# Kernel tuning notes

Hardware: AMD Instinct MI355X
Metric: run time of the kernel (lower is better)

The kernel has to match this reference:

```python
import jax, jax.numpy as jnp
import numpy as np
import math

V = 32000      # vocab_size
D = 1024       # hidden_dims
T_MAX = 1024   # max_txt_len
L = 4          # n_layers
H = 8          # heads (fixed in CausalMHA)
HD = D // H
B, T = 2, 1024
EPS = 1e-5


def setup_inputs() -> dict:
    key = jax.random.key(0)
    ks = jax.random.split(key, 20)
    s = 0.02
    inp = {
        "x": jax.random.randint(ks[0], (B, T), 0, V, dtype=jnp.int64) if jax.config.read("jax_enable_x64") else jax.random.randint(ks[0], (B, T), 0, V, dtype=jnp.int32),
        "tok_emb": jax.random.normal(ks[1], (V, D), jnp.float32) * s,
        "pos_emb": jax.random.normal(ks[2], (1, T_MAX, D), jnp.float32) * s,
        "ln1_g": jnp.ones((L, D), jnp.float32),
        "ln1_b": jnp.zeros((L, D), jnp.float32),
        "wqkv": jax.random.normal(ks[3], (L, D, 3 * D), jnp.float32) * s,
        "bqkv": jnp.zeros((L, 3 * D), jnp.float32),
        "wo": jax.random.normal(ks[4], (L, D, D), jnp.float32) * s,
        "bo": jnp.zeros((L, D), jnp.float32),
        "ln2_g": jnp.ones((L, D), jnp.float32),
        "ln2_b": jnp.zeros((L, D), jnp.float32),
        "wfc": jax.random.normal(ks[5], (L, D, 4 * D), jnp.float32) * s,   # no bias
        "wfc2": jax.random.normal(ks[6], (L, 4 * D, D), jnp.float32) * s,  # no bias
        "fn_g": jnp.ones((D,), jnp.float32),
        "fn_b": jnp.zeros((D,), jnp.float32),
        "wout": jax.random.normal(ks[7], (D, V), jnp.float32) * s,
        "bout": jnp.zeros((V,), jnp.float32),
    }
    return inp


def _ln(x, g, b):
    mu = jnp.mean(x, axis=-1, keepdims=True)
    var = jnp.var(x, axis=-1, keepdims=True)
    return (x - mu) * jax.lax.rsqrt(var + EPS) * g + b


def _attn(xn, wqkv_l, bqkv_l, wo_l, bo_l):
    Bb, Tt, _ = xn.shape
    qkv = xn @ wqkv_l + bqkv_l                      # [B,T,3D]
    q, k, v = jnp.split(qkv, 3, axis=-1)
    q = q.reshape(Bb, Tt, H, HD)
    k = k.reshape(Bb, Tt, H, HD)
    v = v.reshape(Bb, Tt, H, HD)
    scores = jnp.einsum("bqhd,bkhd->bhqk", q, k) / math.sqrt(HD)
    mask = jnp.triu(jnp.ones((Tt, Tt), bool), k=1)   # True above diagonal
    scores = jnp.where(mask, jnp.float32(-jnp.inf), scores)
    att = jax.nn.softmax(scores, axis=-1)
    out = jnp.einsum("bhqk,bkhd->bqhd", att, v).reshape(Bb, Tt, D)
    return out @ wo_l + bo_l


def reference(x, tok_emb, pos_emb, ln1_g, ln1_b, wqkv, bqkv, wo, bo,
              ln2_g, ln2_b, wfc, wfc2, fn_g, fn_b, wout, bout):
    Tt = x.shape[1]
    h = tok_emb[x] + pos_emb[:, :Tt, :]              # [B,T,D]
    for i in range(L):
        h = h + _attn(_ln(h, ln1_g[i], ln1_b[i]), wqkv[i], bqkv[i], wo[i], bo[i])
        hn = _ln(h, ln2_g[i], ln2_b[i])
        h = h + jax.nn.gelu(hn @ wfc[i], approximate=False) @ wfc2[i]
    h = _ln(h, fn_g, fn_b)
    return h @ wout + bout                           # [B,T,V] logits
```

## Files before the change

### kernel.cpp

```cpp
#include <hip/hip_runtime.h>
#include <math.h>
#include <stdint.h>

#define D_  1024
#define T_  1024
#define H_  8
#define HD_ 128
#define L_  4
#define V_  32000
#define M_  2048

typedef __attribute__((ext_vector_type(4))) float f32x4;
typedef __attribute__((ext_vector_type(4))) short s16x4;
typedef __attribute__((ext_vector_type(8))) short s16x8;
typedef unsigned short u16;

__device__ __forceinline__ u16 f2bf(float f) {
  union { float f; uint32_t u; } c; c.f = f;
  uint32_t r = c.u + 0x7fffu + ((c.u >> 16) & 1u);
  return (u16)(r >> 16);
}
__device__ __forceinline__ float bf2f(u16 h) {
  union { uint32_t u; float f; } c; c.u = ((uint32_t)h) << 16;
  return c.f;
}
__device__ __forceinline__ float gelu_f(float x) {
  return 0.5f * x * (1.0f + erff(x * 0.70710678118654752f));
}

__device__ __forceinline__ void gload16(const u16* g, u16* l) {
  __builtin_amdgcn_global_load_lds(
      (const __attribute__((address_space(1))) void*)(uintptr_t)g,
      (__attribute__((address_space(3))) void*)(uint32_t)(uintptr_t)l,
      16, 0, 0);
}

__device__ __forceinline__ void convT_f32_tile(const float* __restrict__ in,
                                               u16* __restrict__ out,
                                               int ldin, int ldout,
                                               int c0, int r0,
                                               u16 (*tile)[72])
{
  const int t = threadIdx.x;
  const int rr = t >> 2, cs = (t & 3) << 4;
  u16 tmp[16];
  const float* p = in + (size_t)(r0 + rr) * ldin + c0 + cs;
#pragma unroll
  for (int q = 0; q < 4; ++q) {
    f32x4 v = *(const f32x4*)(p + q * 4);
#pragma unroll
    for (int j = 0; j < 4; ++j) tmp[q * 4 + j] = f2bf(v[j]);
  }
  *(s16x8*)&tile[rr][cs]     = *(const s16x8*)tmp;
  *(s16x8*)&tile[rr][cs + 8] = *(const s16x8*)(tmp + 8);
  __syncthreads();
  const int cr = t >> 2, rs = (t & 3) << 4;
  u16 o[16];
#pragma unroll
  for (int j = 0; j < 16; ++j) o[j] = tile[rs + j][cr];
  u16* op = out + (size_t)(c0 + cr) * ldout + r0 + rs;
  *(s16x8*)op       = *(const s16x8*)o;
  *(s16x8*)(op + 8) = *(const s16x8*)(o + 8);
}

template<int INF32>
__global__ __launch_bounds__(256)
void convT_kernel(const void* __restrict__ inv, u16* __restrict__ out,
                  int ldin, int ldout, long inZ, long outZ)
{
  __shared__ __align__(16) u16 tile[64][72];
  const int c0 = blockIdx.x << 6, r0 = blockIdx.y << 6;
  if (INF32) {
    convT_f32_tile((const float*)inv + (size_t)blockIdx.z * inZ,
                   out + (size_t)blockIdx.z * outZ, ldin, ldout, c0, r0, tile);
    return;
  }
  const int t = threadIdx.x;
  const int rr = t >> 2, cs = (t & 3) << 4;
  const u16* in = (const u16*)inv + (size_t)blockIdx.z * inZ;
  const u16* p = in + (size_t)(r0 + rr) * ldin + c0 + cs;
  s16x8 v0 = *(const s16x8*)(p);
  s16x8 v1 = *(const s16x8*)(p + 8);
  *(s16x8*)&tile[rr][cs]     = v0;
  *(s16x8*)&tile[rr][cs + 8] = v1;
  __syncthreads();
  const int cr = t >> 2, rs = (t & 3) << 4;
  u16 o[16];
#pragma unroll
  for (int j = 0; j < 16; ++j) o[j] = tile[rs + j][cr];
  u16* op = out + (size_t)blockIdx.z * outZ + (size_t)(c0 + cr) * ldout + r0 + rs;
  *(s16x8*)op       = *(const s16x8*)o;
  *(s16x8*)(op + 8) = *(const s16x8*)(o + 8);
}

__global__ __launch_bounds__(256)
void conv4_kernel(const float* __restrict__ wqkv_l, const float* __restrict__ wo_l,
                  const float* __restrict__ wfc_l, const float* __restrict__ wfc2_l,
                  u16* __restrict__ Wq, u16* __restrict__ Wo,
                  u16* __restrict__ Wf1, u16* __restrict__ Wf2)
{
  __shared__ __align__(16) u16 tile[64][72];
  int f = blockIdx.x;
  if (f < 768) {
    convT_f32_tile(wqkv_l, Wq, 3 * D_, D_, (f % 48) << 6, (f / 48) << 6, tile);
  } else if (f < 1024) {
    f -= 768;
    convT_f32_tile(wo_l, Wo, D_, D_, (f & 15) << 6, (f >> 4) << 6, tile);
  } else if (f < 2048) {
    f -= 1024;
    convT_f32_tile(wfc_l, Wf1, 4 * D_, D_, (f & 63) << 6, (f >> 6) << 6, tile);
  } else {
    f -= 2048;
    convT_f32_tile(wfc2_l, Wf2, D_, 4 * D_, (f & 15) << 6, (f >> 4) << 6, tile);
  }
}

template<int TM, int ACT, int BIAS, int OUT>
__device__ __forceinline__
void gemm2_body(const u16* __restrict__ A, const u16* __restrict__ Bw,
                const float* __restrict__ bias, const float* __restrict__ res,
                void* __restrict__ Cv,
                int K, int lda, int ldb, int ldc, float scale,
                int bx, int by)
{
  constexpr int WN  = (TM == 128) ? 2 : 4;
  constexpr int WNW = 128 / WN;
  constexpr int NJ  = WNW / 16;
  constexpr int AR  = TM / 64;

  const int m0 = bx * TM, n0 = by * 128;
  const int ktiles = K >> 5;

  __shared__ __align__(16) u16 As[2][TM * 32];
  __shared__ __align__(16) u16 Bs[2][128 * 32];

  const int tid = threadIdx.x, lane = tid & 63, wave = tid >> 6;
  const int wm = wave / WN, wn = wave % WN;
  const int l15 = lane & 15, l4 = lane >> 4;
  const int srow = lane >> 2, scol = (lane & 3) << 3;

  f32x4 acc[4][NJ];
  const f32x4 z4 = {0.f, 0.f, 0.f, 0.f};
#pragma unroll
  for (int i = 0; i < 4; ++i)
#pragma unroll
    for (int j = 0; j < NJ; ++j) acc[i][j] = z4;

  auto stage = [&](int kt, int buf) {
    const int kc = (kt << 5) + scol;
#pragma unroll
    for (int r = 0; r < AR; ++r) {
      const int row = r * 64 + wave * 16;
      gload16(A + (size_t)(m0 + row + srow) * lda + kc, &As[buf][row * 32]);
    }
#pragma unroll
    for (int r = 0; r < 2; ++r) {
      const int row = r * 64 + wave * 16;
      gload16(Bw + (size_t)(n0 + row + srow) * ldb + kc, &Bs[buf][row * 32]);
    }
  };

  stage(0, 0);
  __syncthreads();

  for (int kt = 0; kt < ktiles; ++kt) {
    const int buf = kt & 1;
    if (kt + 1 < ktiles) stage(kt + 1, buf ^ 1);
    const u16* ap = &As[buf][(wm * 64 + l15) * 32 + (l4 << 3)];
    const u16* bp = &Bs[buf][(wn * WNW + l15) * 32 + (l4 << 3)];
    s16x8 af[4], bf[NJ];
#pragma unroll
    for (int i = 0; i < 4; ++i) af[i] = *(const s16x8*)(ap + i * (16 * 32));
#pragma unroll
    for (int j = 0; j < NJ; ++j) bf[j] = *(const s16x8*)(bp + j * (16 * 32));
#pragma unroll
    for (int i = 0; i < 4; ++i)
#pragma unroll
      for (int j = 0; j < NJ; ++j)
        acc[i][j] = __builtin_amdgcn_mfma_f32_16x16x32_bf16(af[i], bf[j], acc[i][j], 0, 0, 0);
    __syncthreads();
  }

  float* Cf = (float*)Cv;
  u16*   Ch = (u16*)Cv;
#pragma unroll
  for (int i = 0; i < 4; ++i) {
    const int row0 = m0 + wm * 64 + i * 16 + l4 * 4;
#pragma unroll
    for (int j = 0; j < NJ; ++j) {
      const int col = n0 + wn * WNW + j * 16 + l15;
      const float bv = BIAS ? bias[col] : 0.0f;
#pragma unroll
      for (int r = 0; r < 4; ++r) {
        float v = acc[i][j][r] * scale + bv;
        if (ACT) v = gelu_f(v);
        const size_t idx = (size_t)(row0 + r) * ldc + col;
        if (OUT == 0)      Ch[idx] = f2bf(v);
        else if (OUT == 1) Cf[idx] = v;
        else               Cf[idx] = v + res[idx];
      }
    }
  }
}

__device__ __forceinline__ int2 swz2d() {
  const int gx = gridDim.x, gy = gridDim.y;
  int flat = blockIdx.y * gx + blockIdx.x;
  const int nwg = gx * gy;
  int swz = (flat & 7) * (nwg >> 3) + (flat >> 3);
  return make_int2(swz % gx, swz / gx);
}

__global__ __launch_bounds__(256)
void gemm_qkv(const u16* A, const u16* Bw, const float* bias, void* Cv) {
  int2 b = swz2d();
  gemm2_body<128, 0, 1, 0>(A, Bw, bias, nullptr, Cv, D_, D_, D_, 3 * D_, 1.0f, b.x, b.y);
}
__global__ __launch_bounds__(256)
void gemm_fc1(const u16* A, const u16* Bw, void* Cv) {
  int2 b = swz2d();
  gemm2_body<128, 1, 0, 0>(A, Bw, nullptr, nullptr, Cv, D_, D_, D_, 4 * D_, 1.0f, b.x, b.y);
}
__global__ __launch_bounds__(256)
void gemm_wo(const u16* A, const u16* Bw, const float* bias, const float* res,
             void* Cv) {
  int2 b = swz2d();
  gemm2_body<64, 0, 1, 2>(A, Bw, bias, res, Cv, D_, D_, D_, D_, 1.0f, b.x, b.y);
}
__global__ __launch_bounds__(256)
void gemm_fc2s(const u16* __restrict__ A, const u16* __restrict__ Bw,
               float* __restrict__ P) {
  const int gx = gridDim.x, gy = gridDim.y;
  int flat = (blockIdx.z * gy + blockIdx.y) * gx + blockIdx.x;
  const int nwg = gx * gy * gridDim.z;
  int swz = (flat & 7) * (nwg >> 3) + (flat >> 3);
  const int bx = swz % gx; swz /= gx;
  const int by = swz % gy;
  const int z  = swz / gy;
  gemm2_body<64, 0, 0, 1>(A + z * 1024, Bw + z * 1024, nullptr, nullptr,
                          P + (size_t)z * M_ * D_,
                          1024, 4 * D_, 4 * D_, D_, 1.0f, bx, by);
}
__global__ __launch_bounds__(256)
void reduce4_kernel(const float* __restrict__ P, float* __restrict__ h) {
  const size_t i = (size_t)blockIdx.x * D_ + threadIdx.x * 4;
  f32x4 a = *(const f32x4*)&h[i];
#pragma unroll
  for (int z = 0; z < 4; ++z) {
    f32x4 p = *(const f32x4*)&P[(size_t)z * M_ * D_ + i];
    a[0] += p[0]; a[1] += p[1]; a[2] += p[2]; a[3] += p[3];
  }
  *(f32x4*)&h[i] = a;
}

__global__ __launch_bounds__(512, 2)
void gemm8_logits(const u16* __restrict__ A, const u16* __restrict__ Bw,
                  const float* __restrict__ bias, float* __restrict__ C)
{
  int flat = blockIdx.x;
  int swz = (flat & 7) * 125 + (flat >> 3);
  const int bx = swz & 7;
  const int by = swz >> 3;
  const int m0 = bx << 8, n0 = by << 8;

  __shared__ __align__(16) u16 lds[65536];

  const int tid = threadIdx.x, lane = tid & 63, wave = tid >> 6;
  const int wm = wave >> 2, wn = wave & 3;
  const int l15 = lane & 15, l4 = lane >> 4;

  f32x4 acc[8][4];
  const f32x4 z4 = {0.f, 0.f, 0.f, 0.f};
#pragma unroll
  for (int i = 0; i < 8; ++i)
#pragma unroll
    for (int j = 0; j < 4; ++j) acc[i][j] = z4;

  auto stg = [&](const u16* G, int rowbase, int slot, int kt, int kh) {
    kt = (kt < 15) ? kt : 15;
#pragma unroll
    for (int r = 0; r < 2; ++r) {
      const int u = r * 512 + (wave << 6) + lane;
      const int rw = u >> 2, ks = u & 3;
      const int ksw = ks ^ ((rw >> 1) & 3);
      const u16* src = G + (size_t)(rowbase + rw) * 1024 + (kt << 6) + (kh << 5) + (ksw << 3);
      gload16(src, &lds[slot + r * 4096 + (wave << 9)]);
    }
  };

  s16x8 af[4], bfr[4];

#define LDA4(bb, kk, mh)                                                      \
  {                                                                           \
    _Pragma("unroll") for (int f = 0; f < 4; ++f) {                           \
      const int rw = wm * 128 + (mh) * 64 + f * 16 + l15;                     \
      af[f] = *(const s16x8*)&lds[(bb) + (kk) * 8192 + rw * 32 +              \
                                  ((l4 ^ ((rw >> 1) & 3)) << 3)];             \
    }                                                                         \
  }
#define LDB4(bb, kk)                                                          \
  {                                                                           \
    _Pragma("unroll") for (int f = 0; f < 4; ++f) {                           \
      const int rn = wn * 64 + f * 16 + l15;                                  \
      bfr[f] = *(const s16x8*)&lds[(bb) + 16384 + (kk) * 8192 + rn * 32 +     \
                                   ((l4 ^ ((rn >> 1) & 3)) << 3)];            \
    }                                                                         \
  }
#define MFMA16(mh)                                                            \
  {                                                                           \
    __builtin_amdgcn_s_barrier();                                             \
    asm volatile("s_waitcnt lgkmcnt(0)" ::: "memory");                        \
    __builtin_amdgcn_sched_barrier(0);                                        \
    __builtin_amdgcn_s_setprio(1);                                            \
    _Pragma("unroll") for (int f = 0; f < 4; ++f)                             \
      _Pragma("unroll") for (int nf = 0; nf < 4; ++nf)                        \
        acc[(mh) * 4 + f][nf] = __builtin_amdgcn_mfma_f32_16x16x32_bf16(      \
            af[f], bfr[nf], acc[(mh) * 4 + f][nf], 0, 0, 0);                  \
    __builtin_amdgcn_s_setprio(0);                                            \
  }
#define BAR() __builtin_amdgcn_s_barrier()
#define VM4() asm volatile("s_waitcnt vmcnt(4)" ::: "memory")

  stg(A,  m0, 0,             0, 0);
  stg(Bw, n0, 16384,         0, 0);
  stg(A,  m0, 8192,          0, 1);
  stg(Bw, n0, 16384 + 8192,  0, 1);
  stg(A,  m0, 32768,         1, 0);
  stg(Bw, n0, 32768 + 16384, 1, 0);
  VM4();
  BAR();

  for (int i = 0; i < 8; ++i) {
    const int t = 2 * i;
    LDA4(0, 0, 0); LDB4(0, 0);
    stg(A, m0, 32768 + 8192, t + 1, 1);
    MFMA16(0); BAR();
    LDA4(0, 0, 1);
    stg(Bw, n0, 32768 + 24576, t + 1, 1);
    MFMA16(1); BAR();
    LDA4(0, 1, 0); LDB4(0, 1);
    stg(A, m0, 0, t + 2, 0);
    MFMA16(0); BAR();
    LDA4(0, 1, 1);
    stg(Bw, n0, 16384, t + 2, 0);
    MFMA16(1); VM4(); BAR();
    LDA4(32768, 0, 0); LDB4(32768, 0);
    stg(A, m0, 8192, t + 2, 1);
    MFMA16(0); BAR();
    LDA4(32768, 0, 1);
    stg(Bw, n0, 16384 + 8192, t + 2, 1);
    MFMA16(1); BAR();
    LDA4(32768, 1, 0); LDB4(32768, 1);
    stg(A, m0, 32768, t + 3, 0);
    MFMA16(0); BAR();
    LDA4(32768, 1, 1);
    stg(Bw, n0, 32768 + 16384, t + 3, 0);
    MFMA16(1); VM4(); BAR();
  }
#undef LDA4
#undef LDB4
#undef MFMA16
#undef BAR
#undef VM4

  float bv[4];
#pragma unroll
  for (int nf = 0; nf < 4; ++nf) bv[nf] = bias[n0 + wn * 64 + nf * 16 + l15];
#pragma unroll
  for (int mf = 0; mf < 8; ++mf) {
    const int row0 = m0 + wm * 128 + mf * 16 + l4 * 4;
#pragma unroll
    for (int nf = 0; nf < 4; ++nf) {
      const int col = n0 + wn * 64 + nf * 16 + l15;
#pragma unroll
      for (int r = 0; r < 4; ++r)
        C[(size_t)(row0 + r) * V_ + col] = acc[mf][nf][r] + bv[nf];
    }
  }
}

__global__ __launch_bounds__(256)
void flash_attn(const u16* __restrict__ qkv, const u16* __restrict__ Vt,
                u16* __restrict__ xo)
{
  const int qb = 15 - blockIdx.x;
  const int z  = blockIdx.y;
  const int b  = z >> 3, hh = z & 7;

  __shared__ __align__(16) u16 Ks[64 * 128];
  __shared__ __align__(16) u16 Vs[128 * 64];
  __shared__ __align__(16) u16 Ps[64 * 80];

  const int tid = threadIdx.x, lane = tid & 63, w = tid >> 6;
  const int l15 = lane & 15, l4 = lane >> 4;
  const float iscale = 0.08838834764831845f;

  const int qrow = qb * 64 + w * 16 + l15;
  const u16* qptr = qkv + ((size_t)(b * T_) + qrow) * (3 * D_) + hh * HD_;

  s16x8 bQ[4];
#pragma unroll
  for (int ks = 0; ks < 4; ++ks)
    bQ[ks] = *(const s16x8*)(qptr + ks * 32 + l4 * 8);

  f32x4 O[8];
#pragma unroll
  for (int i = 0; i < 8; ++i) O[i] = {0.f, 0.f, 0.f, 0.f};
  float m_run = -1e30f, l_run = 0.f;

  const int ntiles = qb + 1;
  for (int kt = 0; kt < ntiles; ++kt) {
    __syncthreads();
    {
      const int r = tid >> 2, c = (tid & 3) << 5;
      const u16* src = qkv + ((size_t)(b * T_) + kt * 64 + r) * (3 * D_) + D_ + hh * HD_ + c;
#pragma unroll
      for (int u = 0; u < 4; ++u) {
        s16x8 v = *(const s16x8*)(src + u * 8);
        const int dblk = (c >> 3) + u;
        *(s16x8*)&Ks[r * 128 + ((dblk ^ (r & 7)) << 3)] = v;
      }
      const int d = tid >> 1, kc0 = (tid & 1) << 5;
      const u16* vsrc = Vt + ((size_t)z * HD_ + d) * T_ + kt * 64 + kc0;
#pragma unroll
      for (int u = 0; u < 4; ++u) {
        s16x8 v = *(const s16x8*)(vsrc + u * 8);
        const int kblk = (kc0 >> 3) + u;
        *(s16x8*)&Vs[d * 64 + ((kblk ^ (d & 7)) << 3)] = v;
      }
    }
    __syncthreads();

    f32x4 st[4];
#pragma unroll
    for (int mf = 0; mf < 4; ++mf) st[mf] = {0.f, 0.f, 0.f, 0.f};
#pragma unroll
    for (int ks = 0; ks < 4; ++ks) {
      s16x8 aK[4];
#pragma unroll
      for (int mf = 0; mf < 4; ++mf) {
        const int r = mf * 16 + l15;
        aK[mf] = *(const s16x8*)&Ks[r * 128 + ((((ks << 2) + l4) ^ (r & 7)) << 3)];
      }
#pragma unroll
      for (int mf = 0; mf < 4; ++mf)
        st[mf] = __builtin_amdgcn_mfma_f32_16x16x32_bf16(aK[mf], bQ[ks], st[mf], 0, 0, 0);
    }

    const bool diag = (kt == qb);
    float sv[16];
    float mx = -1e30f;
#pragma unroll
    for (int mf = 0; mf < 4; ++mf)
#pragma unroll
      for (int r = 0; r < 4; ++r) {
        float s = st[mf][r] * iscale;
        if (diag) {
          const int k = kt * 64 + mf * 16 + l4 * 4 + r;
          if (k > qrow) s = -1e30f;
        }
        sv[mf * 4 + r] = s;
        mx = fmaxf(mx, s);
      }
    mx = fmaxf(mx, __shfl_xor(mx, 16));
    mx = fmaxf(mx, __shfl_xor(mx, 32));
    const float m_new = fmaxf(m_run, mx);
    const float sc_old = __expf(m_run - m_new);
    float psum = 0.f;
    u16 pb[16];
#pragma unroll
    for (int j = 0; j < 16; ++j) {
      const float p = __expf(sv[j] - m_new);
      psum += p;
      pb[j] = f2bf(p);
    }
    psum += __shfl_xor(psum, 16);
    psum += __shfl_xor(psum, 32);
    l_run = l_run * sc_old + psum;
    m_run = m_new;

    float scr[4];
#pragma unroll
    for (int r = 0; r < 4; ++r) scr[r] = __shfl(sc_old, l4 * 4 + r);
#pragma unroll
    for (int df = 0; df < 8; ++df)
#pragma unroll
      for (int r = 0; r < 4; ++r) O[df][r] *= scr[r];

    {
      const int row = w * 16 + l15;
#pragma unroll
      for (int j = 0; j < 16; ++j) {
        const int k = (j >> 2) * 16 + l4 * 4 + (j & 3);
        Ps[row * 80 + (((k >> 3) ^ (l15 & 7)) << 3) + (k & 7)] = pb[j];
      }
    }

#pragma unroll
    for (int kc = 0; kc < 2; ++kc) {
      const int prow = w * 16 + l15;
      s16x8 aP = *(const s16x8*)&Ps[prow * 80 + ((((kc << 2) + l4) ^ (l15 & 7)) << 3)];
#pragma unroll
      for (int df = 0; df < 8; ++df) {
        const int d = df * 16 + l15;
        s16x8 bV = *(const s16x8*)&Vs[d * 64 + ((((kc << 2) + l4) ^ (d & 7)) << 3)];
        O[df] = __builtin_amdgcn_mfma_f32_16x16x32_bf16(aP, bV, O[df], 0, 0, 0);
      }
    }
  }

  const float inv_l = 1.0f / l_run;
  float invr[4];
#pragma unroll
  for (int r = 0; r < 4; ++r) invr[r] = __shfl(inv_l, l4 * 4 + r);
#pragma unroll
  for (int df = 0; df < 8; ++df)
#pragma unroll
    for (int r = 0; r < 4; ++r) {
      const int row = qb * 64 + w * 16 + l4 * 4 + r;
      xo[((size_t)(b * T_) + row) * D_ + hh * HD_ + df * 16 + l15] =
          f2bf(O[df][r] * invr[r]);
    }
}

__global__ __launch_bounds__(256)
void ln_bf16(const float* __restrict__ x, const float* __restrict__ g,
             const float* __restrict__ b, u16* __restrict__ y)
{
  __shared__ float red[8];
  const int row = blockIdx.x, tid = threadIdx.x;
  f32x4 v = *(const f32x4*)&x[(size_t)row * D_ + tid * 4];
  float s  = v[0] + v[1] + v[2] + v[3];
  float s2 = v[0]*v[0] + v[1]*v[1] + v[2]*v[2] + v[3]*v[3];
#pragma unroll
  for (int off = 32; off > 0; off >>= 1) {
    s  += __shfl_xor(s, off);
    s2 += __shfl_xor(s2, off);
  }
  if ((tid & 63) == 0) { red[tid >> 6] = s; red[4 + (tid >> 6)] = s2; }
  __syncthreads();
  s  = red[0] + red[1] + red[2] + red[3];
  s2 = red[4] + red[5] + red[6] + red[7];
  const float mean = s * (1.0f / D_);
  const float var  = s2 * (1.0f / D_) - mean * mean;
  const float rs   = rsqrtf(var + 1e-5f);
  f32x4 gg = *(const f32x4*)&g[tid * 4];
  f32x4 bb = *(const f32x4*)&b[tid * 4];
  u16 o[4];
#pragma unroll
  for (int j = 0; j < 4; ++j) o[j] = f2bf((v[j] - mean) * rs * gg[j] + bb[j]);
  *(s16x4*)&y[(size_t)row * D_ + tid * 4] = *(const s16x4*)o;
}

__global__ __launch_bounds__(256)
void embed_kernel(const int* __restrict__ x, const float* __restrict__ tok,
                  const float* __restrict__ pos, float* __restrict__ h)
{
  const int row = blockIdx.x, tid = threadIdx.x;
  const int t = row & (T_ - 1);
  const int id = x[row];
  f32x4 a = *(const f32x4*)&tok[(size_t)id * D_ + tid * 4];
  f32x4 p = *(const f32x4*)&pos[(size_t)t * D_ + tid * 4];
  f32x4 o = {a[0] + p[0], a[1] + p[1], a[2] + p[2], a[3] + p[3]};
  *(f32x4*)&h[(size_t)row * D_ + tid * 4] = o;
}

extern "C" void kernel_launch(void* const* d_in, const int* in_sizes, int n_in,
                              void* d_out, int out_size, void* d_ws, size_t ws_size,
                              hipStream_t stream)
{
  (void)in_sizes; (void)n_in; (void)out_size; (void)ws_size;
  const int*   x     = (const int*)  d_in[0];
  const float* tok   = (const float*)d_in[1];
  const float* pos   = (const float*)d_in[2];
  const float* ln1_g = (const float*)d_in[3];
  const float* ln1_b = (const float*)d_in[4];
  const float* wqkv  = (const float*)d_in[5];
  const float* bqkv  = (const float*)d_in[6];
  const float* wo    = (const float*)d_in[7];
  const float* bo    = (const float*)d_in[8];
  const float* ln2_g = (const float*)d_in[9];
  const float* ln2_b = (const float*)d_in[10];
  const float* wfc   = (const float*)d_in[11];
  const float* wfc2  = (const float*)d_in[12];
  const float* fn_g  = (const float*)d_in[13];
  const float* fn_b  = (const float*)d_in[14];
  const float* wout  = (const float*)d_in[15];
  const float* bout  = (const float*)d_in[16];
  float* out = (float*)d_out;

  float* h  = (float*)d_ws;
  u16* xn   = (u16*)(h + (size_t)M_ * D_);
  u16* Wq   = xn  + (size_t)M_ * D_;
  u16* Wo   = Wq  + (size_t)3 * D_ * D_;
  u16* Wf1  = Wo  + (size_t)D_ * D_;
  u16* Wf2  = Wf1 + (size_t)4 * D_ * D_;
  u16* qkv  = Wf2 + (size_t)4 * D_ * D_;
  u16* Vt   = qkv + (size_t)M_ * 3 * D_;
  u16* S    = Vt  + (size_t)2 * T_ * D_;
  float* P  = (float*)(S + (size_t)M_ * 4 * D_);
  u16* WoutT = Wq;

  embed_kernel<<<M_, 256, 0, stream>>>(x, tok, pos, h);

  for (int l = 0; l < L_; ++l) {
    conv4_kernel<<<3072, 256, 0, stream>>>(
        wqkv + (size_t)l * D_ * 3 * D_, wo + (size_t)l * D_ * D_,
        wfc + (size_t)l * D_ * 4 * D_, wfc2 + (size_t)l * 4 * D_ * D_,
        Wq, Wo, Wf1, Wf2);

    ln_bf16<<<M_, 256, 0, stream>>>(h, ln1_g + l * D_, ln1_b + l * D_, xn);
    gemm_qkv<<<dim3(16, 24), 256, 0, stream>>>(xn, Wq, bqkv + l * 3 * D_, qkv);
    convT_kernel<0><<<dim3(16, 16, 2), 256, 0, stream>>>(
        qkv + 2 * D_, Vt, 3 * D_, T_, (long)T_ * 3 * D_, (long)T_ * D_);
    flash_attn<<<dim3(16, 16), 256, 0, stream>>>(qkv, Vt, xn);
    gemm_wo<<<dim3(32, 8), 256, 0, stream>>>(xn, Wo, bo + l * D_, h, h);
    ln_bf16<<<M_, 256, 0, stream>>>(h, ln2_g + l * D_, ln2_b + l * D_, xn);
    gemm_fc1<<<dim3(16, 32), 256, 0, stream>>>(xn, Wf1, S);
    gemm_fc2s<<<dim3(32, 8, 4), 256, 0, stream>>>(S, Wf2, P);
    reduce4_kernel<<<M_, 256, 0, stream>>>(P, h);
  }

  ln_bf16<<<M_, 256, 0, stream>>>(h, fn_g, fn_b, xn);
  convT_kernel<1><<<dim3(500, 16, 1), 256, 0, stream>>>(
      wout, WoutT, V_, D_, 0, 0);
  gemm8_logits<<<1000, 512, 0, stream>>>(xn, WoutT, bout, out);
}
```

Baseline: 954.9 us.

## Use 8-wave 256x128 pipelined GEMM for MLP and fuse split-K reduce into layernorm

Measured after the change: 895.1 us. 6.3% less time.

```diff
diff --git a/kernel.cpp b/kernel.cpp
--- a/kernel.cpp
+++ b/kernel.cpp
@@ -217,40 +217,144 @@
   gemm2_body<128, 0, 1, 0>(A, Bw, bias, nullptr, Cv, D_, D_, D_, 3 * D_, 1.0f, b.x, b.y);
 }
 __global__ __launch_bounds__(256)
-void gemm_fc1(const u16* A, const u16* Bw, void* Cv) {
-  int2 b = swz2d();
-  gemm2_body<128, 1, 0, 0>(A, Bw, nullptr, nullptr, Cv, D_, D_, D_, 4 * D_, 1.0f, b.x, b.y);
-}
-__global__ __launch_bounds__(256)
 void gemm_wo(const u16* A, const u16* Bw, const float* bias, const float* res,
              void* Cv) {
   int2 b = swz2d();
   gemm2_body<64, 0, 1, 2>(A, Bw, bias, res, Cv, D_, D_, D_, D_, 1.0f, b.x, b.y);
 }
-__global__ __launch_bounds__(256)
-void gemm_fc2s(const u16* __restrict__ A, const u16* __restrict__ Bw,
-               float* __restrict__ P) {
-  const int gx = gridDim.x, gy = gridDim.y;
-  int flat = (blockIdx.z * gy + blockIdx.y) * gx + blockIdx.x;
-  const int nwg = gx * gy * gridDim.z;
-  int swz = (flat & 7) * (nwg >> 3) + (flat >> 3);
-  const int bx = swz % gx; swz /= gx;
-  const int by = swz % gy;
-  const int z  = swz / gy;
-  gemm2_body<64, 0, 0, 1>(A + z * 1024, Bw + z * 1024, nullptr, nullptr,
-                          P + (size_t)z * M_ * D_,
-                          1024, 4 * D_, 4 * D_, D_, 1.0f, bx, by);
-}
-__global__ __launch_bounds__(256)
-void reduce4_kernel(const float* __restrict__ P, float* __restrict__ h) {
-  const size_t i = (size_t)blockIdx.x * D_ + threadIdx.x * 4;
-  f32x4 a = *(const f32x4*)&h[i];
-#pragma unroll
-  for (int z = 0; z < 4; ++z) {
-    f32x4 p = *(const f32x4*)&P[(size_t)z * M_ * D_ + i];
-    a[0] += p[0]; a[1] += p[1]; a[2] += p[2]; a[3] += p[3];
-  }
-  *(f32x4*)&h[i] = a;
+
+template<int OUT, int ACT>
+__device__ __forceinline__
+void gemm8n_body(const u16* __restrict__ A, int lda,
+                 const u16* __restrict__ Bw, int ldb,
+                 void* __restrict__ Cv, int ldc, int bx, int by)
+{
+  const int m0 = bx << 8, n0 = by << 7;
+
+  __shared__ __align__(16) u16 lds[49152];
+
+  const int tid = threadIdx.x, lane = tid & 63, wave = tid >> 6;
+  const int wm = wave >> 1, wn = wave & 1;
+  const int l15 = lane & 15, l4 = lane >> 4;
+
+  f32x4 acc[4][4];
+  const f32x4 z4 = {0.f, 0.f, 0.f, 0.f};
+#pragma unroll
+  for (int i = 0; i < 4; ++i)
+#pragma unroll
+    for (int j = 0; j < 4; ++j) acc[i][j] = z4;
+
+  auto stgA = [&](int buf, int kt, int kh) {
+    kt = (kt < 15) ? kt : 15;
+    const int slot = buf * 24576 + kh * 8192;
+#pragma unroll
+    for (int r = 0; r < 2; ++r) {
+      const int u = r * 512 + (wave << 6) + lane;
+      const int rw = u >> 2, ks = u & 3;
+      const int ksw = ks ^ ((rw >> 1) & 3);
+      gload16(A + (size_t)(m0 + rw) * lda + (kt << 6) + (kh << 5) + (ksw << 3),
+              &lds[slot + r * 4096 + (wave << 9)]);
+    }
+  };
+  auto stgB = [&](int buf, int kt, int kh) {
+    kt = (kt < 15) ? kt : 15;
+    const int slot = buf * 24576 + 16384 + kh * 4096;
+    const int u = (wave << 6) + lane;
+    const int rw = u >> 2, ks = u & 3;
+    const int ksw = ks ^ ((rw >> 1) & 3);
+    gload16(Bw + (size_t)(n0 + rw) * ldb + (kt << 6) + (kh << 5) + (ksw << 3),
+            &lds[slot + (wave << 9)]);
+  };
+
+  s16x8 af[4], bfr[4];
+
+#define LDABN(bb, kk)                                                         \
+  {                                                                           \
+    _Pragma("unroll") for (int f = 0; f < 4; ++f) {                           \
+      const int rw = wm * 64 + f * 16 + l15;                                  \
+      af[f] = *(const s16x8*)&lds[(bb) + (kk) * 8192 + rw * 32 +              \
+                                  ((l4 ^ ((rw >> 1) & 3)) << 3)];             \
+    }                                                                         \
+    _Pragma("unroll") for (int f = 0; f < 4; ++f) {                           \
+      const int rn = wn * 64 + f * 16 + l15;                                  \
+      bfr[f] = *(const s16x8*)&lds[(bb) + 16384 + (kk) * 4096 + rn * 32 +     \
+                                   ((l4 ^ ((rn >> 1) & 3)) << 3)];            \
+    }                                                                         \
+  }
+#define MFMAN()                                                               \
+  {                                                                           \
+    __builtin_amdgcn_s_barrier();                                             \
+    asm volatile("s_waitcnt lgkmcnt(0)" ::: "memory");                        \
+    __builtin_amdgcn_sched_barrier(0);                                        \
+    __builtin_amdgcn_s_setprio(1);                                            \
+    _Pragma("unroll") for (int f = 0; f < 4; ++f)                             \
+      _Pragma("unroll") for (int nf = 0; nf < 4; ++nf)                        \
+        acc[f][nf] = __builtin_amdgcn_mfma_f32_16x16x32_bf16(                 \
+            af[f], bfr[nf], acc[f][nf], 0, 0, 0);                             \
+    __builtin_amdgcn_s_setprio(0);                                            \
+  }
+#define BARN() __builtin_amdgcn_s_barrier()
+#define VM6()  asm volatile("s_waitcnt vmcnt(6)" ::: "memory")
+
+  stgA(0, 0, 0); stgB(0, 0, 0);
+  stgA(0, 0, 1); stgB(0, 0, 1);
+  stgA(1, 1, 0); stgB(1, 1, 0);
+  VM6();
+  BARN();
+
+  for (int i = 0; i < 8; ++i) {
+    const int t = 2 * i;
+    LDABN(0, 0);
+    stgA(1, t + 1, 1); stgB(1, t + 1, 1);
+    MFMAN(); VM6(); BARN();
+    LDABN(0, 1);
+    stgA(0, t + 2, 0); stgB(0, t + 2, 0);
+    MFMAN(); VM6(); BARN();
+    LDABN(24576, 0);
+    stgA(0, t + 2, 1); stgB(0, t + 2, 1);
+    MFMAN(); VM6(); BARN();
+    LDABN(24576, 1);
+    stgA(1, t + 3, 0); stgB(1, t + 3, 0);
+    MFMAN(); VM6(); BARN();
+  }
+#undef LDABN
+#undef MFMAN
+#undef BARN
+#undef VM6
+
+  float* Cf = (float*)Cv;
+  u16*   Ch = (u16*)Cv;
+#pragma unroll
+  for (int mf = 0; mf < 4; ++mf) {
+    const int row0 = m0 + wm * 64 + mf * 16 + l4 * 4;
+#pragma unroll
+    for (int nf = 0; nf < 4; ++nf) {
+      const int col = n0 + wn * 64 + nf * 16 + l15;
+#pragma unroll
+      for (int r = 0; r < 4; ++r) {
+        float v = acc[mf][nf][r];
+        if (ACT) v = gelu_f(v);
+        const size_t idx = (size_t)(row0 + r) * ldc + col;
+        if (OUT == 0) Ch[idx] = f2bf(v);
+        else          Cf[idx] = v;
+      }
+    }
+  }
+}
+
+__global__ __launch_bounds__(512, 1)
+void gemm8n_fc1(const u16* A, const u16* Bw, void* Cv) {
+  int flat = blockIdx.x;
+  int swz = (flat & 7) * 32 + (flat >> 3);
+  gemm8n_body<0, 1>(A, 1024, Bw, 1024, Cv, 4096, swz & 7, swz >> 3);
+}
+__global__ __launch_bounds__(512, 1)
+void gemm8n_fc2(const u16* A, const u16* Bw, float* P) {
+  int flat = blockIdx.x;
+  int swz = (flat & 7) * 32 + (flat >> 3);
+  const int bx = swz & 7, by = (swz >> 3) & 7, z = swz >> 6;
+  gemm8n_body<1, 0>(A + z * 1024, 4096, Bw + z * 1024, 4096,
+                    P + (size_t)z * M_ * D_, 1024, bx, by);
 }
 
 __global__ __launch_bounds__(512, 2)
@@ -524,12 +628,22 @@
 }
 
 __global__ __launch_bounds__(256)
-void ln_bf16(const float* __restrict__ x, const float* __restrict__ g,
-             const float* __restrict__ b, u16* __restrict__ y)
-{
-  __shared__ float red[8];
+void ln_red(float* __restrict__ hbuf, const float* __restrict__ P,
+            const float* __restrict__ g, const float* __restrict__ b,
+            u16* __restrict__ y, int red)
+{
+  __shared__ float red_s[8];
   const int row = blockIdx.x, tid = threadIdx.x;
-  f32x4 v = *(const f32x4*)&x[(size_t)row * D_ + tid * 4];
+  const size_t i = (size_t)row * D_ + tid * 4;
+  f32x4 v = *(const f32x4*)&hbuf[i];
+  if (red) {
+#pragma unroll
+    for (int zp = 0; zp < 4; ++zp) {
+      f32x4 p = *(const f32x4*)&P[(size_t)zp * M_ * D_ + i];
+      v[0] += p[0]; v[1] += p[1]; v[2] += p[2]; v[3] += p[3];
+    }
+    *(f32x4*)&hbuf[i] = v;
+  }
   float s  = v[0] + v[1] + v[2] + v[3];
   float s2 = v[0]*v[0] + v[1]*v[1] + v[2]*v[2] + v[3]*v[3];
 #pragma unroll
@@ -537,10 +651,10 @@
     s  += __shfl_xor(s, off);
     s2 += __shfl_xor(s2, off);
   }
-  if ((tid & 63) == 0) { red[tid >> 6] = s; red[4 + (tid >> 6)] = s2; }
+  if ((tid & 63) == 0) { red_s[tid >> 6] = s; red_s[4 + (tid >> 6)] = s2; }
   __syncthreads();
-  s  = red[0] + red[1] + red[2] + red[3];
-  s2 = red[4] + red[5] + red[6] + red[7];
+  s  = red_s[0] + red_s[1] + red_s[2] + red_s[3];
+  s2 = red_s[4] + red_s[5] + red_s[6] + red_s[7];
   const float mean = s * (1.0f / D_);
   const float var  = s2 * (1.0f / D_) - mean * mean;
   const float rs   = rsqrtf(var + 1e-5f);
@@ -549,7 +663,7 @@
   u16 o[4];
 #pragma unroll
   for (int j = 0; j < 4; ++j) o[j] = f2bf((v[j] - mean) * rs * gg[j] + bb[j]);
-  *(s16x4*)&y[(size_t)row * D_ + tid * 4] = *(const s16x4*)o;
+  *(s16x4*)&y[i] = *(const s16x4*)o;
 }
 
 __global__ __launch_bounds__(256)
@@ -609,19 +723,19 @@
         wfc + (size_t)l * D_ * 4 * D_, wfc2 + (size_t)l * 4 * D_ * D_,
         Wq, Wo, Wf1, Wf2);
 
-    ln_bf16<<<M_, 256, 0, stream>>>(h, ln1_g + l * D_, ln1_b + l * D_, xn);
+    ln_red<<<M_, 256, 0, stream>>>(h, P, ln1_g + l * D_, ln1_b + l * D_, xn,
+                                   l > 0 ? 1 : 0);
     gemm_qkv<<<dim3(16, 24), 256, 0, stream>>>(xn, Wq, bqkv + l * 3 * D_, qkv);
     convT_kernel<0><<<dim3(16, 16, 2), 256, 0, stream>>>(
         qkv + 2 * D_, Vt, 3 * D_, T_, (long)T_ * 3 * D_, (long)T_ * D_);
     flash_attn<<<dim3(16, 16), 256, 0, stream>>>(qkv, Vt, xn);
     gemm_wo<<<dim3(32, 8), 256, 0, stream>>>(xn, Wo, bo + l * D_, h, h);
-    ln_bf16<<<M_, 256, 0, stream>>>(h, ln2_g + l * D_, ln2_b + l * D_, xn);
-    gemm_fc1<<<dim3(16, 32), 256, 0, stream>>>(xn, Wf1, S);
-    gemm_fc2s<<<dim3(32, 8, 4), 256, 0, stream>>>(S, Wf2, P);
-    reduce4_kernel<<<M_, 256, 0, stream>>>(P, h);
-  }
-
-  ln_bf16<<<M_, 256, 0, stream>>>(h, fn_g, fn_b, xn);
+    ln_red<<<M_, 256, 0, stream>>>(h, P, ln2_g + l * D_, ln2_b + l * D_, xn, 0);
+    gemm8n_fc1<<<256, 512, 0, stream>>>(xn, Wf1, S);
+    gemm8n_fc2<<<256, 512, 0, stream>>>(S, Wf2, P);
+  }
+
+  ln_red<<<M_, 256, 0, stream>>>(h, P, fn_g, fn_b, xn, 1);
   convT_kernel<1><<<dim3(500, 16, 1), 256, 0, stream>>>(
       wout, WoutT, V_, D_, 0, 0);
   gemm8_logits<<<1000, 512, 0, stream>>>(xn, WoutT, bout, out);
```
